# Performance work log

Hardware: AMD Instinct MI355X
Metric: run time of the kernel (lower is better)

The kernel has to match this reference:

```python
import jax, jax.numpy as jnp
import numpy as np

ALP = 0.1
LAM = 1.0
N_NODES = 100000
N_EDGES = 800000
D_FEAT = 64


def setup_inputs() -> dict:
    key = jax.random.key(0)
    ks = jax.random.split(key, 7)
    h = jax.random.normal(ks[0], (N_NODES, D_FEAT), dtype=jnp.float32)
    ini_h = jax.random.normal(ks[1], (N_NODES, D_FEAT), dtype=jnp.float32)
    bef_A = jax.random.uniform(ks[2], (N_NODES, 1), dtype=jnp.float32)
    aft_A = jax.random.uniform(ks[3], (N_NODES, 1), dtype=jnp.float32)
    bef_X = jax.random.uniform(ks[4], (N_NODES, 1), dtype=jnp.float32)
    src = jax.random.randint(ks[5], (N_EDGES,), 0, N_NODES, dtype=jnp.int32)
    dst = jax.random.randint(ks[6], (N_EDGES,), 0, N_NODES, dtype=jnp.int32)
    return {"h": h, "ini_h": ini_h, "bef_A": bef_A, "aft_A": aft_A,
            "bef_X": bef_X, "src": src, "dst": dst}


def reference(h, ini_h, bef_A, aft_A, bef_X, src, dst):
    # propagation_lt:
    #   ini_h' = ini_h * bef_X
    #   agg    = A @ (h * aft_A)   (copy_u/sum over edges src->dst)
    #   out    = alp*lam * (agg * bef_A) + (1-alp)*h + alp*ini_h'
    pre_h = h
    msg = (h * aft_A)[src]                                  # [E, D]
    agg = jax.ops.segment_sum(msg, dst, num_segments=N_NODES)  # [N, D]
    agg = agg * bef_A
    return ALP * LAM * agg + (1.0 - ALP) * pre_h + ALP * (ini_h * bef_X)
```

## Files before the change

### kernel.cpp

```cpp
#include <hip/hip_runtime.h>

#define ALP 0.1f
#define OMA 0.9f
#define D 64
#define DV 16
#define SH 9
#define NODES_PER_B 512
#define CAP 16
#define OVF_MAX 65536

__device__ __forceinline__ unsigned short f2b(float f) {
    unsigned u = __float_as_uint(f);
    unsigned r = u + 0x7fffu + ((u >> 16) & 1u);
    return (unsigned short)(r >> 16);
}
__device__ __forceinline__ float b2f(unsigned short u) {
    return __uint_as_float(((unsigned)u) << 16);
}

__global__ void vsgc_msg(const float4* __restrict__ h4, const float* __restrict__ aft_A,
                         ushort4* __restrict__ msgb, int n16) {
    int i = blockIdx.x * blockDim.x + threadIdx.x;
    if (i >= n16) return;
    float w = aft_A[i >> 4];
    float4 v = h4[i];
    msgb[i] = make_ushort4(f2b(v.x * w), f2b(v.y * w), f2b(v.z * w), f2b(v.w * w));
}

__global__ __launch_bounds__(256) void p1_scatter(const int4* __restrict__ src4,
                                                  const int4* __restrict__ dst4,
                                                  int* __restrict__ gcnt,
                                                  int* __restrict__ buckets,
                                                  int2* __restrict__ ovf,
                                                  int* __restrict__ ovfCnt,
                                                  int E, int NB, int BCAP) {
    __shared__ int cnt[256], gbase[256], pos[256];
    int tid = threadIdx.x;
    cnt[tid] = 0; pos[tid] = 0;
    __syncthreads();
    int nInt4 = (E + 3) >> 2;
    int i0 = blockIdx.x * 512 + tid;
    int i1 = i0 + 256;
    bool v0 = i0 < nInt4, v1 = i1 < nInt4;
    int4 s0 = make_int4(0,0,0,0), d0 = s0, s1 = s0, d1 = s0;
    if (v0) { s0 = src4[i0]; d0 = dst4[i0]; }
    if (v1) { s1 = src4[i1]; d1 = dst4[i1]; }
    int e0 = i0 << 2, e1 = i1 << 2;
    if (v0) {
        if (e0 + 0 < E) atomicAdd(&cnt[d0.x >> SH], 1);
        if (e0 + 1 < E) atomicAdd(&cnt[d0.y >> SH], 1);
        if (e0 + 2 < E) atomicAdd(&cnt[d0.z >> SH], 1);
        if (e0 + 3 < E) atomicAdd(&cnt[d0.w >> SH], 1);
    }
    if (v1) {
        if (e1 + 0 < E) atomicAdd(&cnt[d1.x >> SH], 1);
        if (e1 + 1 < E) atomicAdd(&cnt[d1.y >> SH], 1);
        if (e1 + 2 < E) atomicAdd(&cnt[d1.z >> SH], 1);
        if (e1 + 3 < E) atomicAdd(&cnt[d1.w >> SH], 1);
    }
    __syncthreads();
    if (tid < NB && cnt[tid] > 0) gbase[tid] = atomicAdd(&gcnt[tid], cnt[tid]);
    __syncthreads();
#define EMIT(ss, dd, ok)                                                        \
    if (ok) {                                                                   \
        int b = (dd) >> SH;                                                     \
        int p = gbase[b] + atomicAdd(&pos[b], 1);                               \
        int pkt = ((ss) << SH) | ((dd) & (NODES_PER_B - 1));                    \
        if (p < BCAP) buckets[(size_t)b * BCAP + p] = pkt;                      \
        else { int o = atomicAdd(ovfCnt, 1); if (o < OVF_MAX) ovf[o] = make_int2(ss, dd); } \
    }
    EMIT(s0.x, d0.x, v0 && e0 + 0 < E)
    EMIT(s0.y, d0.y, v0 && e0 + 1 < E)
    EMIT(s0.z, d0.z, v0 && e0 + 2 < E)
    EMIT(s0.w, d0.w, v0 && e0 + 3 < E)
    EMIT(s1.x, d1.x, v1 && e1 + 0 < E)
    EMIT(s1.y, d1.y, v1 && e1 + 1 < E)
    EMIT(s1.z, d1.z, v1 && e1 + 2 < E)
    EMIT(s1.w, d1.w, v1 && e1 + 3 < E)
#undef EMIT
}

__global__ __launch_bounds__(512) void p2_ell(const int* __restrict__ buckets,
                                              const int* __restrict__ gcnt,
                                              int* __restrict__ ell,
                                              int* __restrict__ cnt_g,
                                              int2* __restrict__ ovf,
                                              int* __restrict__ ovfCnt,
                                              int N, int BCAP) {
    __shared__ int npos[NODES_PER_B];
    int b = blockIdx.x, tid = threadIdx.x;
    npos[tid] = 0;
    __syncthreads();
    int nb = min(gcnt[b], BCAP);
    const int* bp = buckets + (size_t)b * BCAP;
    for (int i = tid; i < nb; i += 512) {
        int pkt = bp[i];
        int l = pkt & (NODES_PER_B - 1);
        int s = (int)(((unsigned)pkt) >> SH);
        int slot = atomicAdd(&npos[l], 1);
        int node = (b << SH) + l;
        if (slot < CAP) ell[(size_t)node * CAP + slot] = s;
        else { int o = atomicAdd(ovfCnt, 1); if (o < OVF_MAX) ovf[o] = make_int2(s, node); }
    }
    __syncthreads();
    int node = (b << SH) + tid;
    if (node < N) cnt_g[node] = npos[tid];
}

__global__ __launch_bounds__(256) void vsgc_gather_ell(const ushort4* __restrict__ msgb,
                                                       const float4* __restrict__ h4,
                                                       const float4* __restrict__ ini4,
                                                       const float* __restrict__ bef_A,
                                                       const float* __restrict__ bef_X,
                                                       const int* __restrict__ cnt_g,
                                                       const int* __restrict__ ell,
                                                       float4* __restrict__ out4, int N) {
    int g = (blockIdx.x * blockDim.x + threadIdx.x) >> 6;
    if (g >= N) return;
    int lane = threadIdx.x & 63;
    int w = lane >> 4;
    int q = lane & 15;
    int ev = ell[(size_t)g * CAP + q];
    int n = min(cnt_g[g], CAP);
    float4 acc = make_float4(0.f, 0.f, 0.f, 0.f);
#pragma unroll
    for (int k = 0; k < 4; ++k) {
        int idx = w + 4 * k;
        int s = __shfl(ev, idx);
        if (idx < n) {
            ushort4 m = msgb[(size_t)s * DV + q];
            acc.x += b2f(m.x);
            acc.y += b2f(m.y);
            acc.z += b2f(m.z);
            acc.w += b2f(m.w);
        }
    }
    acc.x += __shfl_xor(acc.x, 16); acc.y += __shfl_xor(acc.y, 16);
    acc.z += __shfl_xor(acc.z, 16); acc.w += __shfl_xor(acc.w, 16);
    acc.x += __shfl_xor(acc.x, 32); acc.y += __shfl_xor(acc.y, 32);
    acc.z += __shfl_xor(acc.z, 32); acc.w += __shfl_xor(acc.w, 32);
    if (w == 0) {
        float cb = ALP * bef_A[g];
        float bx = ALP * bef_X[g];
        size_t idx = (size_t)g * DV + q;
        float4 hv = h4[idx];
        float4 iv = ini4[idx];
        float4 o;
        o.x = OMA * hv.x + bx * iv.x + cb * acc.x;
        o.y = OMA * hv.y + bx * iv.y + cb * acc.y;
        o.z = OMA * hv.z + bx * iv.z + cb * acc.z;
        o.w = OMA * hv.w + bx * iv.w + cb * acc.w;
        out4[idx] = o;
    }
}

__global__ void vsgc_ovf(const float4* __restrict__ h4,
                         const float* __restrict__ aft_A,
                         const float* __restrict__ bef_A,
                         const int2* __restrict__ ovf,
                         const int* __restrict__ ovfCnt,
                         float* __restrict__ out) {
    int total = min(*ovfCnt, OVF_MAX);
    int stride = blockDim.x * gridDim.x;
    for (int t = blockIdx.x * blockDim.x + threadIdx.x; t < total * 16; t += stride) {
        int e = t >> 4, q = t & 15;
        int2 r = ovf[e];
        float c = ALP * aft_A[r.x] * bef_A[r.y];
        float4 hv = h4[(size_t)r.x * DV + q];
        float* op = out + (size_t)r.y * D + (q << 2);
        unsafeAtomicAdd(op + 0, c * hv.x);
        unsafeAtomicAdd(op + 1, c * hv.y);
        unsafeAtomicAdd(op + 2, c * hv.z);
        unsafeAtomicAdd(op + 3, c * hv.w);
    }
}

__global__ void vsgc_init(const float4* __restrict__ h, const float4* __restrict__ ini_h,
                          const float* __restrict__ bef_X, float4* __restrict__ out, int n4) {
    int i = blockIdx.x * blockDim.x + threadIdx.x;
    if (i >= n4) return;
    int node = i >> 4;
    float bx = ALP * bef_X[node];
    float4 hv = h[i];
    float4 iv = ini_h[i];
    float4 o;
    o.x = OMA * hv.x + bx * iv.x;
    o.y = OMA * hv.y + bx * iv.y;
    o.z = OMA * hv.z + bx * iv.z;
    o.w = OMA * hv.w + bx * iv.w;
    out[i] = o;
}
__global__ void vsgc_edges_atomic(const float4* __restrict__ h,
                                  const float* __restrict__ aft_A,
                                  const float* __restrict__ bef_A,
                                  const int* __restrict__ src,
                                  const int* __restrict__ dst,
                                  float* __restrict__ out, int E) {
    int tid = blockIdx.x * blockDim.x + threadIdx.x;
    int e = tid >> 4;
    int q = tid & 15;
    if (e >= E) return;
    int s = src[e];
    int d = dst[e];
    float c = ALP * aft_A[s] * bef_A[d];
    float4 hv = h[(size_t)s * DV + q];
    float* op = out + (size_t)d * D + (q << 2);
    unsafeAtomicAdd(op + 0, c * hv.x);
    unsafeAtomicAdd(op + 1, c * hv.y);
    unsafeAtomicAdd(op + 2, c * hv.z);
    unsafeAtomicAdd(op + 3, c * hv.w);
}

extern "C" void kernel_launch(void* const* d_in, const int* in_sizes, int n_in,
                              void* d_out, int out_size, void* d_ws, size_t ws_size,
                              hipStream_t stream) {
    const float* h     = (const float*)d_in[0];
    const float* ini_h = (const float*)d_in[1];
    const float* bef_A = (const float*)d_in[2];
    const float* aft_A = (const float*)d_in[3];
    const float* bef_X = (const float*)d_in[4];
    const int*   src   = (const int*)d_in[5];
    const int*   dst   = (const int*)d_in[6];
    float* out = (float*)d_out;

    const int N = in_sizes[0] / D;
    const int E = in_sizes[5];
    const int t = 256;

    int NB = (N + NODES_PER_B - 1) >> SH;
    int perB = (NB > 0) ? E / NB : 0;
    int BCAP = perB + perB / 4 + 256;

    size_t o_gcnt = 0;
    size_t o_ovfc = 256 * 4;
    size_t o_ovf  = ((o_ovfc + 64 * 4 + 255) / 256) * 256;
    size_t o_cnt  = o_ovf + (size_t)OVF_MAX * 8;
    size_t o_ell  = ((o_cnt + (size_t)N * 4 + 255) / 256) * 256;
    size_t o_bkt  = ((o_ell + (size_t)N * CAP * 4 + 255) / 256) * 256;
    size_t o_msg  = ((o_bkt + (size_t)NB * BCAP * 4 + 255) / 256) * 256;
    size_t need   = o_msg + (size_t)N * 128;

    if (NB <= 256 && N <= (1 << (31 - SH)) && ws_size >= need) {
        int*  gcnt  = (int*)((char*)d_ws + o_gcnt);
        int*  ovfC  = (int*)((char*)d_ws + o_ovfc);
        int2* ovf   = (int2*)((char*)d_ws + o_ovf);
        int*  cnt_g = (int*)((char*)d_ws + o_cnt);
        int*  ell   = (int*)((char*)d_ws + o_ell);
        int*  bkt   = (int*)((char*)d_ws + o_bkt);
        ushort4* msgb = (ushort4*)((char*)d_ws + o_msg);

        hipMemsetAsync(d_ws, 0, o_ovf, stream);

        int n16 = N * DV;
        vsgc_msg<<<(n16 + t - 1) / t, t, 0, stream>>>((const float4*)h, aft_A, msgb, n16);

        int nInt4 = (E + 3) >> 2;
        int p1blocks = (nInt4 + 511) / 512;
        p1_scatter<<<p1blocks, 256, 0, stream>>>(
            (const int4*)src, (const int4*)dst, gcnt, bkt, ovf, ovfC, E, NB, BCAP);

        p2_ell<<<NB, 512, 0, stream>>>(bkt, gcnt, ell, cnt_g, ovf, ovfC, N, BCAP);

        long long threadsTotal = (long long)N * 64;
        vsgc_gather_ell<<<(int)((threadsTotal + t - 1) / t), t, 0, stream>>>(
            msgb, (const float4*)h, (const float4*)ini_h, bef_A, bef_X,
            cnt_g, ell, (float4*)out, N);

        vsgc_ovf<<<64, t, 0, stream>>>((const float4*)h, aft_A, bef_A, ovf, ovfC, out);
    } else {
        int n4 = N * DV;
        vsgc_init<<<(n4 + t - 1) / t, t, 0, stream>>>(
            (const float4*)h, (const float4*)ini_h, bef_X, (float4*)out, n4);
        long long total = (long long)E * DV;
        vsgc_edges_atomic<<<(int)((total + t - 1) / t), t, 0, stream>>>(
            (const float4*)h, aft_A, bef_A, src, dst, out, E);
    }
}
```

Measured before the change: 168.4 us.

## Fold workspace memset into msg kernel and vectorize bucket and gather loads

Removes the separate hipMemsetAsync by having block 0 of the message kernel zero the counter region. The scatter pass is restructured to issue all shared-memory position atomics before the global stores, and p2_ell now reads packets as int4 with BCAP rounded to a multiple of four. The gather kernel hoists the h, ini_h and coefficient loads above the edge loop and replaces the divergent edge branch with clamped, masked unconditional loads. The overflow kernel grid is halved. The masked loads fetch message rows even for empty ELL slots, which adds memory traffic for low-degree nodes.

```diff
diff --git a/kernel.cpp b/kernel.cpp
--- a/kernel.cpp
+++ b/kernel.cpp
@@ -19,7 +19,11 @@
 }
 
 __global__ void vsgc_msg(const float4* __restrict__ h4, const float* __restrict__ aft_A,
-                         ushort4* __restrict__ msgb, int n16) {
+                         ushort4* __restrict__ msgb, int* __restrict__ zeroRegion,
+                         int zeroWords, int n16) {
+    if (blockIdx.x == 0) {
+        for (int j = threadIdx.x; j < zeroWords; j += blockDim.x) zeroRegion[j] = 0;
+    }
     int i = blockIdx.x * blockDim.x + threadIdx.x;
     if (i >= n16) return;
     float w = aft_A[i >> 4];
@@ -46,38 +50,28 @@
     if (v0) { s0 = src4[i0]; d0 = dst4[i0]; }
     if (v1) { s1 = src4[i1]; d1 = dst4[i1]; }
     int e0 = i0 << 2, e1 = i1 << 2;
-    if (v0) {
-        if (e0 + 0 < E) atomicAdd(&cnt[d0.x >> SH], 1);
-        if (e0 + 1 < E) atomicAdd(&cnt[d0.y >> SH], 1);
-        if (e0 + 2 < E) atomicAdd(&cnt[d0.z >> SH], 1);
-        if (e0 + 3 < E) atomicAdd(&cnt[d0.w >> SH], 1);
-    }
-    if (v1) {
-        if (e1 + 0 < E) atomicAdd(&cnt[d1.x >> SH], 1);
-        if (e1 + 1 < E) atomicAdd(&cnt[d1.y >> SH], 1);
-        if (e1 + 2 < E) atomicAdd(&cnt[d1.z >> SH], 1);
-        if (e1 + 3 < E) atomicAdd(&cnt[d1.w >> SH], 1);
-    }
+    int ss[8] = {s0.x, s0.y, s0.z, s0.w, s1.x, s1.y, s1.z, s1.w};
+    int dd[8] = {d0.x, d0.y, d0.z, d0.w, d1.x, d1.y, d1.z, d1.w};
+    bool ok[8];
+#pragma unroll
+    for (int k = 0; k < 4; ++k) { ok[k] = v0 && (e0 + k < E); ok[4 + k] = v1 && (e1 + k < E); }
+#pragma unroll
+    for (int k = 0; k < 8; ++k) if (ok[k]) atomicAdd(&cnt[dd[k] >> SH], 1);
     __syncthreads();
     if (tid < NB && cnt[tid] > 0) gbase[tid] = atomicAdd(&gcnt[tid], cnt[tid]);
     __syncthreads();
-#define EMIT(ss, dd, ok)                                                        \
-    if (ok) {                                                                   \
-        int b = (dd) >> SH;                                                     \
-        int p = gbase[b] + atomicAdd(&pos[b], 1);                               \
-        int pkt = ((ss) << SH) | ((dd) & (NODES_PER_B - 1));                    \
-        if (p < BCAP) buckets[(size_t)b * BCAP + p] = pkt;                      \
-        else { int o = atomicAdd(ovfCnt, 1); if (o < OVF_MAX) ovf[o] = make_int2(ss, dd); } \
-    }
-    EMIT(s0.x, d0.x, v0 && e0 + 0 < E)
-    EMIT(s0.y, d0.y, v0 && e0 + 1 < E)
-    EMIT(s0.z, d0.z, v0 && e0 + 2 < E)
-    EMIT(s0.w, d0.w, v0 && e0 + 3 < E)
-    EMIT(s1.x, d1.x, v1 && e1 + 0 < E)
-    EMIT(s1.y, d1.y, v1 && e1 + 1 < E)
-    EMIT(s1.z, d1.z, v1 && e1 + 2 < E)
-    EMIT(s1.w, d1.w, v1 && e1 + 3 < E)
-#undef EMIT
+    int pp[8];
+#pragma unroll
+    for (int k = 0; k < 8; ++k)
+        pp[k] = ok[k] ? (gbase[dd[k] >> SH] + atomicAdd(&pos[dd[k] >> SH], 1)) : 0;
+#pragma unroll
+    for (int k = 0; k < 8; ++k) {
+        if (!ok[k]) continue;
+        int b = dd[k] >> SH;
+        int pkt = (ss[k] << SH) | (dd[k] & (NODES_PER_B - 1));
+        if (pp[k] < BCAP) buckets[(size_t)b * BCAP + pp[k]] = pkt;
+        else { int o = atomicAdd(ovfCnt, 1); if (o < OVF_MAX) ovf[o] = make_int2(ss[k], dd[k]); }
+    }
 }
 
 __global__ __launch_bounds__(512) void p2_ell(const int* __restrict__ buckets,
@@ -92,15 +86,23 @@
     npos[tid] = 0;
     __syncthreads();
     int nb = min(gcnt[b], BCAP);
-    const int* bp = buckets + (size_t)b * BCAP;
-    for (int i = tid; i < nb; i += 512) {
-        int pkt = bp[i];
-        int l = pkt & (NODES_PER_B - 1);
-        int s = (int)(((unsigned)pkt) >> SH);
-        int slot = atomicAdd(&npos[l], 1);
-        int node = (b << SH) + l;
-        if (slot < CAP) ell[(size_t)node * CAP + slot] = s;
-        else { int o = atomicAdd(ovfCnt, 1); if (o < OVF_MAX) ovf[o] = make_int2(s, node); }
+    const int4* bp4 = (const int4*)(buckets + (size_t)b * BCAP);
+    int nIter = (nb + 3) >> 2;
+    for (int i4 = tid; i4 < nIter; i4 += 512) {
+        int4 r4 = bp4[i4];
+        int base = i4 << 2;
+        int pk[4] = {r4.x, r4.y, r4.z, r4.w};
+#pragma unroll
+        for (int k = 0; k < 4; ++k) {
+            if (base + k >= nb) break;
+            int pkt = pk[k];
+            int l = pkt & (NODES_PER_B - 1);
+            int s = (int)(((unsigned)pkt) >> SH);
+            int slot = atomicAdd(&npos[l], 1);
+            int node = (b << SH) + l;
+            if (slot < CAP) ell[(size_t)node * CAP + slot] = s;
+            else { int o = atomicAdd(ovfCnt, 1); if (o < OVF_MAX) ovf[o] = make_int2(s, node); }
+        }
     }
     __syncthreads();
     int node = (b << SH) + tid;
@@ -120,37 +122,37 @@
     int lane = threadIdx.x & 63;
     int w = lane >> 4;
     int q = lane & 15;
+    size_t ridx = (size_t)g * DV + q;
     int ev = ell[(size_t)g * CAP + q];
     int n = min(cnt_g[g], CAP);
+    float4 hv = h4[ridx];
+    float4 iv = ini4[ridx];
+    float cb = ALP * bef_A[g];
+    float bx = ALP * bef_X[g];
     float4 acc = make_float4(0.f, 0.f, 0.f, 0.f);
 #pragma unroll
     for (int k = 0; k < 4; ++k) {
         int idx = w + 4 * k;
         int s = __shfl(ev, idx);
-        if (idx < n) {
-            ushort4 m = msgb[(size_t)s * DV + q];
-            acc.x += b2f(m.x);
-            acc.y += b2f(m.y);
-            acc.z += b2f(m.z);
-            acc.w += b2f(m.w);
-        }
+        unsigned su = min((unsigned)s, (unsigned)(N - 1));
+        float m = (idx < n) ? 1.f : 0.f;
+        ushort4 mm = msgb[(size_t)su * DV + q];
+        acc.x += m * b2f(mm.x);
+        acc.y += m * b2f(mm.y);
+        acc.z += m * b2f(mm.z);
+        acc.w += m * b2f(mm.w);
     }
     acc.x += __shfl_xor(acc.x, 16); acc.y += __shfl_xor(acc.y, 16);
     acc.z += __shfl_xor(acc.z, 16); acc.w += __shfl_xor(acc.w, 16);
     acc.x += __shfl_xor(acc.x, 32); acc.y += __shfl_xor(acc.y, 32);
     acc.z += __shfl_xor(acc.z, 32); acc.w += __shfl_xor(acc.w, 32);
     if (w == 0) {
-        float cb = ALP * bef_A[g];
-        float bx = ALP * bef_X[g];
-        size_t idx = (size_t)g * DV + q;
-        float4 hv = h4[idx];
-        float4 iv = ini4[idx];
         float4 o;
         o.x = OMA * hv.x + bx * iv.x + cb * acc.x;
         o.y = OMA * hv.y + bx * iv.y + cb * acc.y;
         o.z = OMA * hv.z + bx * iv.z + cb * acc.z;
         o.w = OMA * hv.w + bx * iv.w + cb * acc.w;
-        out4[idx] = o;
+        out4[ridx] = o;
     }
 }
 
@@ -229,7 +231,7 @@
 
     int NB = (N + NODES_PER_B - 1) >> SH;
     int perB = (NB > 0) ? E / NB : 0;
-    int BCAP = perB + perB / 4 + 256;
+    int BCAP = ((perB + perB / 4 + 256) + 3) & ~3;
 
     size_t o_gcnt = 0;
     size_t o_ovfc = 256 * 4;
@@ -249,10 +251,10 @@
         int*  bkt   = (int*)((char*)d_ws + o_bkt);
         ushort4* msgb = (ushort4*)((char*)d_ws + o_msg);
 
-        hipMemsetAsync(d_ws, 0, o_ovf, stream);
-
+        int zeroWords = (int)(o_ovf / 4);
         int n16 = N * DV;
-        vsgc_msg<<<(n16 + t - 1) / t, t, 0, stream>>>((const float4*)h, aft_A, msgb, n16);
+        vsgc_msg<<<(n16 + t - 1) / t, t, 0, stream>>>(
+            (const float4*)h, aft_A, msgb, (int*)d_ws, zeroWords, n16);
 
         int nInt4 = (E + 3) >> 2;
         int p1blocks = (nInt4 + 511) / 512;
@@ -266,7 +268,7 @@
             msgb, (const float4*)h, (const float4*)ini_h, bef_A, bef_X,
             cnt_g, ell, (float4*)out, N);
 
-        vsgc_ovf<<<64, t, 0, stream>>>((const float4*)h, aft_A, bef_A, ovf, ovfC, out);
+        vsgc_ovf<<<32, t, 0, stream>>>((const float4*)h, aft_A, bef_A, ovf, ovfC, out);
     } else {
         int n4 = N * DV;
         vsgc_init<<<(n4 + t - 1) / t, t, 0, stream>>>(
```

New measurement: 162.5 us. 1.04x faster.
